# Optimization experiments

Hardware: AMD Instinct MI355X
Metric: run time of the kernel (lower is better)

## Reference

```python
import jax, jax.numpy as jnp
import numpy as np

N_NODES = 100000
N_EDGES = 1600000
N_GRAPHS = 64
IN_F, HID, OUT_F = 10, 128, 101


def setup_inputs() -> dict:
    key = jax.random.key(0)
    ks = jax.random.split(key, 12)
    x = jax.random.normal(ks[0], (N_NODES, IN_F), dtype=jnp.float32)
    edge_index = jax.random.randint(ks[1], (2, N_EDGES), 0, N_NODES, dtype=jnp.int64)
    batch = jnp.sort(jax.random.randint(ks[2], (N_NODES,), 0, N_GRAPHS, dtype=jnp.int64))
    def lin(k, fi, fo):
        s = 1.0 / np.sqrt(fi)
        return jax.random.uniform(k, (fi, fo), minval=-s, maxval=s, dtype=jnp.float32)
    W1 = lin(ks[3], IN_F, HID); b1 = jnp.zeros((HID,), jnp.float32)
    W2 = lin(ks[4], HID, HID); b2 = jnp.zeros((HID,), jnp.float32)
    W3 = lin(ks[5], HID, HID); b3 = jnp.zeros((HID,), jnp.float32)
    Wl = lin(ks[6], HID, OUT_F)
    bl = jax.random.uniform(ks[7], (OUT_F,), minval=-1/np.sqrt(HID), maxval=1/np.sqrt(HID), dtype=jnp.float32)
    return {"x": x, "edge_index": edge_index, "batch": batch,
            "W1": W1, "b1": b1, "W2": W2, "b2": b2, "W3": W3, "b3": b3,
            "Wl": Wl, "bl": bl}


def _gcn_norm(edge_index, n_nodes):
    # Add self-loops and compute symmetric normalization (PyG gcn_norm).
    loop = jnp.arange(n_nodes, dtype=edge_index.dtype)
    src = jnp.concatenate([edge_index[0], loop])
    dst = jnp.concatenate([edge_index[1], loop])
    deg = jax.ops.segment_sum(jnp.ones_like(dst, dtype=jnp.float32), dst, num_segments=n_nodes)
    dis = jnp.where(deg > 0, jax.lax.rsqrt(deg), 0.0)
    w = dis[src] * dis[dst]  # [E + N]
    return src, dst, w


def _gcn_conv(x, W, b, src, dst, w, n_nodes):
    h = x @ W                      # transform first (matches GCNConv)
    msg = h[src] * w[:, None]      # gather + edge normalize
    out = jax.ops.segment_sum(msg, dst, num_segments=n_nodes)  # scatter-add
    return out + b


def reference(x, edge_index, batch, W1, b1, W2, b2, W3, b3, Wl, bl):
    n = x.shape[0]
    src, dst, w = _gcn_norm(edge_index, n)
    h = jax.nn.relu(_gcn_conv(x, W1, b1, src, dst, w, n))
    h = jax.nn.relu(_gcn_conv(h, W2, b2, src, dst, w, n))
    h = _gcn_conv(h, W3, b3, src, dst, w, n)
    # global mean pool per graph
    sums = jax.ops.segment_sum(h, batch, num_segments=N_GRAPHS)
    cnts = jax.ops.segment_sum(jnp.ones((n,), jnp.float32), batch, num_segments=N_GRAPHS)
    pooled = sums / jnp.maximum(cnts, 1.0)[:, None]
    # dropout is identity in eval mode
    return pooled @ Wl + bl
```

## Files before the change

kernel.cpp:

```cpp
#include <hip/hip_runtime.h>
#include <hip/hip_bf16.h>
#include <hip/hip_fp16.h>

#define HID 128
#define OUTF 101
#define INF 10

#define BUCK_SHIFT 8
#define NBUCK_MAX 512
#define BCAP 4608
#define BS_TPB 256
#define BS_EPT 32
#define BS_EPB (BS_TPB * BS_EPT)
#define FS_TPB 512
#define FS_EPT 9

typedef __hip_bfloat16 bf16;
typedef __attribute__((ext_vector_type(8))) short short8;
typedef __attribute__((ext_vector_type(4))) float f32x4;
typedef __attribute__((ext_vector_type(2))) float f32x2;

__device__ __forceinline__ float bflo(unsigned u) { return __uint_as_float(u << 16); }
__device__ __forceinline__ float bfhi(unsigned u) { return __uint_as_float(u & 0xffff0000u); }
__device__ __forceinline__ f32x2 bfv(unsigned u) {
    f32x2 r;
    r.x = __uint_as_float(u << 16);
    r.y = __uint_as_float(u & 0xffff0000u);
    return r;
}
__device__ __forceinline__ unsigned pk2(float a, float b) {
    __hip_bfloat162 t;
    t.x = __float2bfloat16(a);
    t.y = __float2bfloat16(b);
    return *reinterpret_cast<unsigned*>(&t);
}
__device__ __forceinline__ float2 h2f2(unsigned u) {
    __half2 h = *reinterpret_cast<__half2*>(&u);
    return __half22float2(h);
}
__device__ __forceinline__ unsigned f2h2(float a, float b) {
    __half2 h = __floats2half2_rn(a, b);
    return *reinterpret_cast<unsigned*>(&h);
}


__device__ __forceinline__ void wsplit_body(const float* __restrict__ W, bf16* __restrict__ wfh,
                                            bf16* __restrict__ wfl, int t) {
    int j    = t & 7;
    int lane = (t >> 3) & 63;
    int nt   = (t >> 9) & 7;
    int kb   = t >> 12;
    int k  = kb * 32 + (lane >> 4) * 8 + j;
    int nn = nt * 16 + (lane & 15);
    float w = W[k * HID + nn];
    float hi = __bfloat162float(__float2bfloat16(w));
    wfh[t] = __float2bfloat16(hi);
    wfl[t] = __float2bfloat16(w - hi);
}

__global__ void prep_kernel(const float* __restrict__ W2, bf16* __restrict__ wf2h,
                            bf16* __restrict__ wf2l,
                            const float* __restrict__ W3, bf16* __restrict__ wf3h,
                            bf16* __restrict__ wf3l,
                            int* __restrict__ gcur, int nbuck,
                            float* __restrict__ sums, int sums_n,
                            unsigned* __restrict__ xps_dummy,
                            unsigned* __restrict__ hs_dummy)
{
    int b = blockIdx.x;
    int tid = threadIdx.x;
    if (b < 64) { wsplit_body(W2, wf2h, wf2l, b * 256 + tid); return; }
    b -= 64;
    if (b < 64) { wsplit_body(W3, wf3h, wf3l, b * 256 + tid); return; }
    b -= 64;
    if (b == 0) {
        for (int k = tid; k < nbuck; k += 256) gcur[k] = k * BCAP;
        return;
    }
    b -= 1;
    if (b < 8) {
        int t = b * 256 + tid;
        if (t * 4 < sums_n) ((float4*)sums)[t] = make_float4(0.f, 0.f, 0.f, 0.f);
        return;
    }
    if (tid < 8) xps_dummy[tid] = 0u;
    if (tid < 64) hs_dummy[tid] = 0u;
}


__global__ __launch_bounds__(BS_TPB) void bucket_scatter_kernel(
        const int* __restrict__ src, const int* __restrict__ dst, int E,
        int* __restrict__ gcur, int* __restrict__ estage, int nbuck) {
    __shared__ int cnt[NBUCK_MAX];
    __shared__ int base[NBUCK_MAX];
    int tid = threadIdx.x;
    int e0 = blockIdx.x * BS_EPB + tid;
    int ds[BS_EPT], ss[BS_EPT];
#pragma unroll
    for (int t = 0; t < BS_EPT; ++t) {
        int e = e0 + t * BS_TPB;
        ds[t] = (e < E) ? dst[e] : -1;
        ss[t] = (e < E) ? src[e] : 0;
    }
    for (int b = tid; b < NBUCK_MAX; b += BS_TPB) cnt[b] = 0;
    __syncthreads();
#pragma unroll
    for (int t = 0; t < BS_EPT; ++t)
        if (ds[t] >= 0) atomicAdd(&cnt[ds[t] >> BUCK_SHIFT], 1);
    __syncthreads();
    for (int b = tid; b < nbuck; b += BS_TPB) {
        int c = cnt[b];
        base[b] = c ? atomicAdd(&gcur[b], c) : 0;
    }
    __syncthreads();
    for (int b = tid; b < NBUCK_MAX; b += BS_TPB) cnt[b] = 0;
    __syncthreads();
#pragma unroll
    for (int t = 0; t < BS_EPT; ++t)
        if (ds[t] >= 0) {
            int bk = ds[t] >> BUCK_SHIFT;
            int o = atomicAdd(&cnt[bk], 1);
            estage[base[bk] + o] = ss[t] | ((ds[t] & 255) << 20);
        }
}

__global__ __launch_bounds__(FS_TPB) void fine_scatter_kernel(
        const int* __restrict__ estage, const int* __restrict__ gcur,
        float* __restrict__ dis, int* __restrict__ rowp,
        int* __restrict__ csrs, const float* __restrict__ x,
        unsigned* __restrict__ xps, int n, int nbuck) {
    __shared__ int sh[FS_TPB];
    __shared__ int hist[256];
    __shared__ int pfx[256];
    __shared__ int lcur[256];
    __shared__ float sdis[256];
    int b = blockIdx.x;
    int tid = threadIdx.x;

    sh[tid] = (tid < nbuck) ? (gcur[tid] - tid * BCAP) : 0;
    __syncthreads();
    for (int off = 1; off < FS_TPB; off <<= 1) {
        int v = (tid >= off) ? sh[tid - off] : 0;
        __syncthreads();
        sh[tid] += v;
        __syncthreads();
    }
    int bb = (b == 0) ? 0 : sh[b - 1];
    int cnt = sh[b] - bb;
    if (b == 0 && tid == 0) rowp[n] = sh[nbuck - 1];

    int node_lo = b << BUCK_SHIFT;
    int slo = b * BCAP;
    int regs[FS_EPT];
#pragma unroll
    for (int t = 0; t < FS_EPT; ++t) {
        int k = tid + t * FS_TPB;
        regs[t] = (k < cnt) ? estage[slo + k] : -1;
    }
    if (tid < 256) hist[tid] = 0;
    __syncthreads();
#pragma unroll
    for (int t = 0; t < FS_EPT; ++t)
        if (regs[t] >= 0) atomicAdd(&hist[(regs[t] >> 20) & 255], 1);
    __syncthreads();
    if (tid < 256) {
        int deg = hist[tid];
        int node = node_lo + tid;
        float dv = rsqrtf((float)(deg + 1));
        sdis[tid] = dv;
        if (node < n) dis[node] = dv;
        pfx[tid] = deg;
    }
    __syncthreads();
    for (int off = 1; off < 256; off <<= 1) {
        int v = 0;
        if (tid < 256 && tid >= off) v = pfx[tid - off];
        __syncthreads();
        if (tid < 256 && tid >= off) pfx[tid] += v;
        __syncthreads();
    }
    if (tid < 256) {
        int excl = (tid == 0) ? 0 : pfx[tid - 1];
        int node = node_lo + tid;
        if (node < n) rowp[node] = bb + excl;
        lcur[tid] = excl;
    }
    __syncthreads();
#pragma unroll
    for (int t = 0; t < FS_EPT; ++t)
        if (regs[t] >= 0) {
            int pos = bb + atomicAdd(&lcur[(regs[t] >> 20) & 255], 1);
            csrs[pos] = regs[t] & 0xFFFFF;
        }
#pragma unroll
    for (int t = 0; t < 4; ++t) {
        int idx = tid + t * FS_TPB;
        int nd = node_lo + (idx >> 3);
        int d = idx & 7;
        if (nd < n) {
            float dvn = sdis[idx >> 3];
            float v0 = (2 * d < INF) ? x[(size_t)nd * INF + 2 * d] * dvn : 0.f;
            float v1 = (2 * d + 1 < INF) ? x[(size_t)nd * INF + 2 * d + 1] * dvn : 0.f;
            xps[(size_t)nd * 8 + d] = f2h2(v0, v1);
        }
    }
}

__global__ __launch_bounds__(256) void aggxform10_kernel(
        const unsigned* __restrict__ xps, const int* __restrict__ rowp,
        const int* __restrict__ csrs, const float* __restrict__ dis,
        const float* __restrict__ W1, const float* __restrict__ b1,
        bf16* __restrict__ h, int n) {
    int i = blockIdx.x * 4 + (threadIdx.x >> 6);
    if (i >= n) return;
    int lane = threadIdx.x & 63;
    int slot = lane >> 3;
    int f = lane & 7;
    float dd = dis[i];

    float acc0, acc1;
    if (slot == 0) {
        float2 v = h2f2(xps[(size_t)i * 8 + f]);
        acc0 = v.x; acc1 = v.y;
    } else {
        acc0 = acc1 = 0.f;
    }

    int beg = rowp[i];
    int end = rowp[i + 1];
    for (int base = beg; base < end; base += 16) {
        int e0 = base + slot;
        int e1 = base + 8 + slot;
        int i0 = (e0 < end) ? e0 : end - 1;
        int i1 = (e1 < end) ? e1 : end - 1;
        int s0 = csrs[i0];
        int s1 = csrs[i1];
        s0 = (e0 < end) ? s0 : n;
        s1 = (e1 < end) ? s1 : n;
        float2 v0 = h2f2(xps[(size_t)s0 * 8 + f]);
        float2 v1 = h2f2(xps[(size_t)s1 * 8 + f]);
        acc0 += v0.x + v1.x;
        acc1 += v0.y + v1.y;
    }
    acc0 += __shfl_xor(acc0, 8, 64);
    acc0 += __shfl_xor(acc0, 16, 64);
    acc0 += __shfl_xor(acc0, 32, 64);
    acc1 += __shfl_xor(acc1, 8, 64);
    acc1 += __shfl_xor(acc1, 16, 64);
    acc1 += __shfl_xor(acc1, 32, 64);
    acc0 *= dd;
    acc1 *= dd;

    float axk[INF];
#pragma unroll
    for (int k = 0; k < INF; ++k) axk[k] = __shfl((k & 1) ? acc1 : acc0, k >> 1, 8);

    int j0 = 2 * lane;
    float2 bb = *(const float2*)(b1 + j0);
    float r0 = bb.x, r1 = bb.y;
#pragma unroll
    for (int k = 0; k < INF; ++k) {
        float2 wv = *(const float2*)(W1 + k * HID + j0);
        r0 = fmaf(axk[k], wv.x, r0);
        r1 = fmaf(axk[k], wv.y, r1);
    }
    r0 = fmaxf(r0, 0.f);
    r1 = fmaxf(r1, 0.f);
    ((unsigned*)(h + (size_t)i * HID))[lane] = pk2(r0, r1);
}

__global__ __launch_bounds__(256) void lin128_mfma_kernel(
        const bf16* __restrict__ in, const bf16* __restrict__ wfh,
        const bf16* __restrict__ wfl, const float* __restrict__ dis,
        bf16* __restrict__ out, int n) {
    __shared__ short8 wh[2048];
    __shared__ short8 wl[2048];
    for (int v = threadIdx.x; v < 2048; v += 256) {
        wh[v] = ((const short8*)wfh)[v];
        wl[v] = ((const short8*)wfl)[v];
    }
    __syncthreads();

    int lane = threadIdx.x & 63;
    int wave = threadIdx.x >> 6;
    int col = lane & 15;
    int quad = lane >> 4;
    int m0 = blockIdx.x * 128 + wave * 32;

    f32x4 acc[2][8];
#pragma unroll
    for (int mt = 0; mt < 2; ++mt)
#pragma unroll
        for (int nt = 0; nt < 8; ++nt) acc[mt][nt] = (f32x4){0.f, 0.f, 0.f, 0.f};

    long rmax = n - 1;
    long r0 = m0 + col;        if (r0 > rmax) r0 = rmax;
    long r1 = m0 + 16 + col;   if (r1 > rmax) r1 = rmax;

#pragma unroll
    for (int kb = 0; kb < 4; ++kb) {
        int kofs = kb * 32 + quad * 8;
        short8 a0 = *(const short8*)(in + r0 * HID + kofs);
        short8 a1 = *(const short8*)(in + r1 * HID + kofs);
        int bbase = kb * 512 + lane;
#pragma unroll
        for (int nt = 0; nt < 8; ++nt) {
            short8 bh = wh[bbase + nt * 64];
            short8 bl = wl[bbase + nt * 64];
            acc[0][nt] = __builtin_amdgcn_mfma_f32_16x16x32_bf16(a0, bh, acc[0][nt], 0, 0, 0);
            acc[1][nt] = __builtin_amdgcn_mfma_f32_16x16x32_bf16(a1, bh, acc[1][nt], 0, 0, 0);
            acc[0][nt] = __builtin_amdgcn_mfma_f32_16x16x32_bf16(a0, bl, acc[0][nt], 0, 0, 0);
            acc[1][nt] = __builtin_amdgcn_mfma_f32_16x16x32_bf16(a1, bl, acc[1][nt], 0, 0, 0);
        }
    }

#pragma unroll
    for (int mt = 0; mt < 2; ++mt) {
        int mb = m0 + mt * 16 + quad * 4;
#pragma unroll
        for (int r = 0; r < 4; ++r) {
            int m = mb + r;
            if (m < n) {
                float dm = dis[m];
                bf16* orow = out + (size_t)m * HID + col;
#pragma unroll
                for (int nt = 0; nt < 8; ++nt)
                    orow[nt * 16] = __float2bfloat16(acc[mt][nt][r] * dm);
            }
        }
    }
}

__global__ __launch_bounds__(256) void agg128_kernel(
        const bf16* __restrict__ hs, const int* __restrict__ rowp,
        const int* __restrict__ csrs, const float* __restrict__ dis,
        const float* __restrict__ b, bf16* __restrict__ out, int n, int relu) {
    int i = blockIdx.x * 4 + (threadIdx.x >> 6);
    if (i >= n) return;
    int lane = threadIdx.x & 63;
    int slot = lane >> 4;
    int f = lane & 15;
    float dd = dis[i];

    f32x2 acc[4];
    if (slot == 0) {
        uint4 v = *(const uint4*)(hs + (size_t)i * HID + f * 8);
        acc[0] = bfv(v.x); acc[1] = bfv(v.y); acc[2] = bfv(v.z); acc[3] = bfv(v.w);
    } else {
#pragma unroll
        for (int j = 0; j < 4; ++j) acc[j] = (f32x2){0.f, 0.f};
    }

    int beg = rowp[i];
    int end = rowp[i + 1];
    for (int base = beg; base < end; base += 16) {
        int s[4];
#pragma unroll
        for (int u = 0; u < 4; ++u) {
            int e = base + u * 4 + slot;
            int idx = (e < end) ? e : end - 1;
            int sv = csrs[idx];
            s[u] = (e < end) ? sv : n;
        }
        uint4 v[4];
#pragma unroll
        for (int u = 0; u < 4; ++u) v[u] = *(const uint4*)(hs + (size_t)s[u] * HID + f * 8);
#pragma unroll
        for (int u = 0; u < 4; ++u) {
            acc[0] += bfv(v[u].x);
            acc[1] += bfv(v[u].y);
            acc[2] += bfv(v[u].z);
            acc[3] += bfv(v[u].w);
        }
    }

    float a[8];
    a[0] = acc[0].x; a[1] = acc[0].y; a[2] = acc[1].x; a[3] = acc[1].y;
    a[4] = acc[2].x; a[5] = acc[2].y; a[6] = acc[3].x; a[7] = acc[3].y;
#pragma unroll
    for (int j = 0; j < 8; ++j) {
        a[j] += __shfl_xor(a[j], 16, 64);
        a[j] += __shfl_xor(a[j], 32, 64);
    }

    float4 b0 = *(const float4*)(b + f * 8);
    float4 b1 = *(const float4*)(b + f * 8 + 4);
    float r[8];
    r[0] = fmaf(a[0], dd, b0.x); r[1] = fmaf(a[1], dd, b0.y);
    r[2] = fmaf(a[2], dd, b0.z); r[3] = fmaf(a[3], dd, b0.w);
    r[4] = fmaf(a[4], dd, b1.x); r[5] = fmaf(a[5], dd, b1.y);
    r[6] = fmaf(a[6], dd, b1.z); r[7] = fmaf(a[7], dd, b1.w);
    if (relu) {
#pragma unroll
        for (int j = 0; j < 8; ++j) r[j] = fmaxf(r[j], 0.f);
    }
    if (slot == 0) {
        uint4 pk;
        pk.x = pk2(r[0], r[1]);
        pk.y = pk2(r[2], r[3]);
        pk.z = pk2(r[4], r[5]);
        pk.w = pk2(r[6], r[7]);
        *(uint4*)(out + (size_t)i * HID + f * 8) = pk;
    }
}

__global__ __launch_bounds__(64) void pool_kernel(const bf16* __restrict__ h,
                                                  const int* __restrict__ batch, int n,
                                                  float* __restrict__ sums) {
    int g = blockIdx.x;
    int t = threadIdx.x;
    int lo = 0, hi = n;
    while (lo < hi) { int mid = (lo + hi) >> 1; if (batch[mid] < g) lo = mid + 1; else hi = mid; }
    int start = lo;
    lo = start; hi = n;
    while (lo < hi) { int mid = (lo + hi) >> 1; if (batch[mid] < g + 1) lo = mid + 1; else hi = mid; }
    int end = lo;
    f32x2 a = (f32x2){0.f, 0.f};
    for (int i = start + blockIdx.y; i < end; i += gridDim.y)
        a += bfv(((const unsigned*)h)[(size_t)i * 64 + t]);
    atomicAdd(&sums[g * HID + 2 * t], a.x);
    atomicAdd(&sums[g * HID + 2 * t + 1], a.y);
}

__global__ void final_kernel(const float* __restrict__ sums, const int* __restrict__ batch, int n,
                             const float* __restrict__ Wl, const float* __restrict__ bl,
                             float* __restrict__ out) {
    int g = blockIdx.x;
    int o = threadIdx.x;
    __shared__ float p[HID];
    int lo = 0, hi = n;
    while (lo < hi) { int mid = (lo + hi) >> 1; if (batch[mid] < g) lo = mid + 1; else hi = mid; }
    int start = lo;
    lo = start; hi = n;
    while (lo < hi) { int mid = (lo + hi) >> 1; if (batch[mid] < g + 1) lo = mid + 1; else hi = mid; }
    float cnt = fmaxf((float)(lo - start), 1.0f);
    p[o] = sums[g * HID + o] / cnt;
    __syncthreads();
    if (o < OUTF) {
        float acc = bl[o];
#pragma unroll 8
        for (int k = 0; k < HID; ++k) acc += p[k] * Wl[k * OUTF + o];
        out[g * OUTF + o] = acc;
    }
}


extern "C" void kernel_launch(void* const* d_in, const int* in_sizes, int n_in,
                              void* d_out, int out_size, void* d_ws, size_t ws_size,
                              hipStream_t stream) {
    const float* x   = (const float*)d_in[0];
    const int*   ei  = (const int*)d_in[1];
    const int*   bat = (const int*)d_in[2];
    const float* W1  = (const float*)d_in[3];
    const float* b1  = (const float*)d_in[4];
    const float* W2  = (const float*)d_in[5];
    const float* b2  = (const float*)d_in[6];
    const float* W3  = (const float*)d_in[7];
    const float* b3  = (const float*)d_in[8];
    const float* Wl  = (const float*)d_in[9];
    const float* bl  = (const float*)d_in[10];

    const int N = in_sizes[0] / INF;
    const int E = in_sizes[1] / 2;
    const int G = out_size / OUTF;
    const int* src = ei;
    const int* dst = ei + E;

    const int nbuck = (N + (1 << BUCK_SHIFT) - 1) >> BUCK_SHIFT;

    char* w = (char*)d_ws;
    bf16*  bufA   = (bf16*)w;  w += (size_t)(N + 1) * HID * 2;
    bf16*  bufB   = (bf16*)w;  w += (size_t)(N + 1) * HID * 2;
    float* dis    = (float*)w; w += (size_t)N * 4;
    int*   rowp   = (int*)w;   w += (size_t)(N + 8) * 4;
    int*   csrs   = (int*)w;   w += (size_t)E * 4;
    float* sums   = (float*)w; w += (size_t)G * HID * 4;
    int*   gcur   = (int*)w;   w += (size_t)(nbuck + 8) * 4;
    bf16*  wf2h   = (bf16*)w;  w += (size_t)HID * HID * 2;
    bf16*  wf2l   = (bf16*)w;  w += (size_t)HID * HID * 2;
    bf16*  wf3h   = (bf16*)w;  w += (size_t)HID * HID * 2;
    bf16*  wf3l   = (bf16*)w;  w += (size_t)HID * HID * 2;
    int*      estage = (int*)bufA;
    unsigned* xps    = (unsigned*)bufB;

    const int sums_n = G * HID;
    prep_kernel<<<64 + 64 + 1 + 8 + 1, 256, 0, stream>>>(
        W2, wf2h, wf2l, W3, wf3h, wf3l, gcur, nbuck, sums, sums_n,
        xps + (size_t)N * 8, (unsigned*)(bufB + (size_t)N * HID));

    bucket_scatter_kernel<<<(E + BS_EPB - 1) / BS_EPB, BS_TPB, 0, stream>>>(src, dst, E, gcur,
                                                                            estage, nbuck);
    fine_scatter_kernel<<<nbuck, FS_TPB, 0, stream>>>(estage, gcur, dis, rowp, csrs, x, xps,
                                                      N, nbuck);

    aggxform10_kernel<<<(N + 3) / 4, 256, 0, stream>>>(xps, rowp, csrs, dis, W1, b1, bufA, N);
    lin128_mfma_kernel<<<(N + 127) / 128, 256, 0, stream>>>(bufA, wf2h, wf2l, dis, bufB, N);
    agg128_kernel<<<(N + 3) / 4, 256, 0, stream>>>(bufB, rowp, csrs, dis, b2, bufA, N, 1);
    lin128_mfma_kernel<<<(N + 127) / 128, 256, 0, stream>>>(bufA, wf3h, wf3l, dis, bufB, N);
    agg128_kernel<<<(N + 3) / 4, 256, 0, stream>>>(bufB, rowp, csrs, dis, b3, bufA, N, 0);

    pool_kernel<<<dim3(G, 32), 64, 0, stream>>>(bufA, bat, N, sums);
    final_kernel<<<G, HID, 0, stream>>>(sums, bat, N, Wl, bl, (float*)d_out);
}
```

Before: 353.0 us.

## Pack 16 nodes per block in first-layer aggregate and split agg128 launches

The first-layer aggregate+transform kernel now handles 16 nodes per 256-thread block instead of 4. Each node gets 16 threads that walk its edges two at a time, and the aggregated 10-feature vector is staged in shared memory so every thread computes 8 output channels with float4 weight loads. This cuts idle lanes for low-degree nodes but adds a block barrier. The agg128 kernel also gains a node offset and count, and each layer's aggregation is launched as two half-range kernels. That split mostly adds launch overhead without visible overlap on the same stream.

Measured after the change: 353.4 us. About the same (+0.1%).

```diff
diff --git a/kernel.cpp b/kernel.cpp
--- a/kernel.cpp
+++ b/kernel.cpp
@@ -211,62 +211,60 @@
         const int* __restrict__ csrs, const float* __restrict__ dis,
         const float* __restrict__ W1, const float* __restrict__ b1,
         bf16* __restrict__ h, int n) {
-    int i = blockIdx.x * 4 + (threadIdx.x >> 6);
+    __shared__ float axs[16][10];
+    int t = threadIdx.x;
+    int ni = t >> 4;
+    int sub = t & 15;
+    int slot = sub >> 3;
+    int d = sub & 7;
+    int i = blockIdx.x * 16 + ni;
+    int iq = (i < n) ? i : n - 1;
+
+    float dd = dis[iq];
+    float acc0 = 0.f, acc1 = 0.f;
+    if (slot == 0) {
+        float2 v = h2f2(xps[(size_t)iq * 8 + d]);
+        acc0 = v.x; acc1 = v.y;
+    }
+    int beg = rowp[iq];
+    int end = rowp[iq + 1];
+    for (int k = beg + slot; k < end; k += 2) {
+        int s = csrs[k];
+        float2 v = h2f2(xps[(size_t)s * 8 + d]);
+        acc0 += v.x;
+        acc1 += v.y;
+    }
+    acc0 += __shfl_xor(acc0, 8, 64);
+    acc1 += __shfl_xor(acc1, 8, 64);
+    if (slot == 0 && d < 5) {
+        axs[ni][2 * d]     = acc0 * dd;
+        axs[ni][2 * d + 1] = acc1 * dd;
+    }
+    __syncthreads();
     if (i >= n) return;
-    int lane = threadIdx.x & 63;
-    int slot = lane >> 3;
-    int f = lane & 7;
-    float dd = dis[i];
-
-    float acc0, acc1;
-    if (slot == 0) {
-        float2 v = h2f2(xps[(size_t)i * 8 + f]);
-        acc0 = v.x; acc1 = v.y;
-    } else {
-        acc0 = acc1 = 0.f;
-    }
-
-    int beg = rowp[i];
-    int end = rowp[i + 1];
-    for (int base = beg; base < end; base += 16) {
-        int e0 = base + slot;
-        int e1 = base + 8 + slot;
-        int i0 = (e0 < end) ? e0 : end - 1;
-        int i1 = (e1 < end) ? e1 : end - 1;
-        int s0 = csrs[i0];
-        int s1 = csrs[i1];
-        s0 = (e0 < end) ? s0 : n;
-        s1 = (e1 < end) ? s1 : n;
-        float2 v0 = h2f2(xps[(size_t)s0 * 8 + f]);
-        float2 v1 = h2f2(xps[(size_t)s1 * 8 + f]);
-        acc0 += v0.x + v1.x;
-        acc1 += v0.y + v1.y;
-    }
-    acc0 += __shfl_xor(acc0, 8, 64);
-    acc0 += __shfl_xor(acc0, 16, 64);
-    acc0 += __shfl_xor(acc0, 32, 64);
-    acc1 += __shfl_xor(acc1, 8, 64);
-    acc1 += __shfl_xor(acc1, 16, 64);
-    acc1 += __shfl_xor(acc1, 32, 64);
-    acc0 *= dd;
-    acc1 *= dd;
-
-    float axk[INF];
-#pragma unroll
-    for (int k = 0; k < INF; ++k) axk[k] = __shfl((k & 1) ? acc1 : acc0, k >> 1, 8);
-
-    int j0 = 2 * lane;
-    float2 bb = *(const float2*)(b1 + j0);
-    float r0 = bb.x, r1 = bb.y;
+
+    int j0 = sub * 8;
+    float ax[INF];
+#pragma unroll
+    for (int k = 0; k < INF; ++k) ax[k] = axs[ni][k];
+    float4 bb0 = *(const float4*)(b1 + j0);
+    float4 bb1 = *(const float4*)(b1 + j0 + 4);
+    float r[8] = {bb0.x, bb0.y, bb0.z, bb0.w, bb1.x, bb1.y, bb1.z, bb1.w};
 #pragma unroll
     for (int k = 0; k < INF; ++k) {
-        float2 wv = *(const float2*)(W1 + k * HID + j0);
-        r0 = fmaf(axk[k], wv.x, r0);
-        r1 = fmaf(axk[k], wv.y, r1);
-    }
-    r0 = fmaxf(r0, 0.f);
-    r1 = fmaxf(r1, 0.f);
-    ((unsigned*)(h + (size_t)i * HID))[lane] = pk2(r0, r1);
+        float4 w0 = *(const float4*)(W1 + k * HID + j0);
+        float4 w1 = *(const float4*)(W1 + k * HID + j0 + 4);
+        r[0] = fmaf(ax[k], w0.x, r[0]); r[1] = fmaf(ax[k], w0.y, r[1]);
+        r[2] = fmaf(ax[k], w0.z, r[2]); r[3] = fmaf(ax[k], w0.w, r[3]);
+        r[4] = fmaf(ax[k], w1.x, r[4]); r[5] = fmaf(ax[k], w1.y, r[5]);
+        r[6] = fmaf(ax[k], w1.z, r[6]); r[7] = fmaf(ax[k], w1.w, r[7]);
+    }
+    uint4 pk;
+    pk.x = pk2(fmaxf(r[0], 0.f), fmaxf(r[1], 0.f));
+    pk.y = pk2(fmaxf(r[2], 0.f), fmaxf(r[3], 0.f));
+    pk.z = pk2(fmaxf(r[4], 0.f), fmaxf(r[5], 0.f));
+    pk.w = pk2(fmaxf(r[6], 0.f), fmaxf(r[7], 0.f));
+    *(uint4*)(h + (size_t)i * HID + j0) = pk;
 }
 
 __global__ __launch_bounds__(256) void lin128_mfma_kernel(
@@ -334,9 +332,11 @@
 __global__ __launch_bounds__(256) void agg128_kernel(
         const bf16* __restrict__ hs, const int* __restrict__ rowp,
         const int* __restrict__ csrs, const float* __restrict__ dis,
-        const float* __restrict__ b, bf16* __restrict__ out, int n, int relu) {
-    int i = blockIdx.x * 4 + (threadIdx.x >> 6);
-    if (i >= n) return;
+        const float* __restrict__ b, bf16* __restrict__ out, int n, int relu,
+        int node0, int ncnt) {
+    int local = blockIdx.x * 4 + (threadIdx.x >> 6);
+    if (local >= ncnt) return;
+    int i = node0 + local;
     int lane = threadIdx.x & 63;
     int slot = lane >> 4;
     int f = lane & 15;
@@ -493,11 +493,19 @@
     fine_scatter_kernel<<<nbuck, FS_TPB, 0, stream>>>(estage, gcur, dis, rowp, csrs, x, xps,
                                                       N, nbuck);
 
-    aggxform10_kernel<<<(N + 3) / 4, 256, 0, stream>>>(xps, rowp, csrs, dis, W1, b1, bufA, N);
+    aggxform10_kernel<<<(N + 15) / 16, 256, 0, stream>>>(xps, rowp, csrs, dis, W1, b1, bufA, N);
+
+    const int half = (N + 1) / 2;
     lin128_mfma_kernel<<<(N + 127) / 128, 256, 0, stream>>>(bufA, wf2h, wf2l, dis, bufB, N);
-    agg128_kernel<<<(N + 3) / 4, 256, 0, stream>>>(bufB, rowp, csrs, dis, b2, bufA, N, 1);
+    agg128_kernel<<<(half + 3) / 4, 256, 0, stream>>>(bufB, rowp, csrs, dis, b2, bufA, N, 1,
+                                                      0, half);
+    agg128_kernel<<<(N - half + 3) / 4, 256, 0, stream>>>(bufB, rowp, csrs, dis, b2, bufA, N, 1,
+                                                          half, N - half);
     lin128_mfma_kernel<<<(N + 127) / 128, 256, 0, stream>>>(bufA, wf3h, wf3l, dis, bufB, N);
-    agg128_kernel<<<(N + 3) / 4, 256, 0, stream>>>(bufB, rowp, csrs, dis, b3, bufA, N, 0);
+    agg128_kernel<<<(half + 3) / 4, 256, 0, stream>>>(bufB, rowp, csrs, dis, b3, bufA, N, 0,
+                                                      0, half);
+    agg128_kernel<<<(N - half + 3) / 4, 256, 0, stream>>>(bufB, rowp, csrs, dis, b3, bufA, N, 0,
+                                                          half, N - half);
 
     pool_kernel<<<dim3(G, 32), 64, 0, stream>>>(bufA, bat, N, sums);
     final_kernel<<<G, HID, 0, stream>>>(sums, bat, N, Wl, bl, (float*)d_out);
```
